# Optimization experiments

Measured on AMD Instinct MI355X. Metric: run time of the kernel, lower is better.

The kernel has to match this reference:

```python
import jax, jax.numpy as jnp
import numpy as np

N_NODES = 50000
N_EDGES = 800000


def sage_conv(x, src, dst, W_l, W_r, b):
    # PyG SAGEConv (mean aggr): out = lin_l(mean_{j->i} x_j) + lin_r(x_i)
    msg_sum = jax.ops.segment_sum(x[src], dst, num_segments=N_NODES)  # [N, d]
    deg = jax.ops.segment_sum(jnp.ones((src.shape[0],), x.dtype), dst,
                              num_segments=N_NODES)
    agg = msg_sum / jnp.clip(deg, 1.0)[:, None]
    return agg @ W_l.T + x @ W_r.T + b


def setup_inputs() -> dict:
    key = jax.random.key(0)
    ks = jax.random.split(key, 8)
    in_dim, hid, out_dim = 128, 256, 128
    x = jax.random.normal(ks[0], (N_NODES, in_dim), dtype=jnp.float32)
    edge_index = jax.random.randint(ks[1], (2, N_EDGES), 0, N_NODES, dtype=jnp.int64)
    s1 = 1.0 / np.sqrt(in_dim)
    s2 = 1.0 / np.sqrt(hid)
    return {
        "x": x,
        "edge_index": edge_index,
        "W_l1": jax.random.uniform(ks[2], (hid, in_dim), jnp.float32, -s1, s1),
        "W_r1": jax.random.uniform(ks[3], (hid, in_dim), jnp.float32, -s1, s1),
        "b1": jnp.zeros((hid,), jnp.float32),
        "W_l2": jax.random.uniform(ks[4], (out_dim, hid), jnp.float32, -s2, s2),
        "W_r2": jax.random.uniform(ks[5], (out_dim, hid), jnp.float32, -s2, s2),
        "b2": jnp.zeros((out_dim,), jnp.float32),
    }


def reference(x, edge_index, W_l1, W_r1, b1, W_l2, W_r2, b2):
    src, dst = edge_index[0], edge_index[1]
    h = sage_conv(x, src, dst, W_l1, W_r1, b1)
    h = jax.nn.relu(h)
    # dropout is identity in eval mode
    out = sage_conv(h, src, dst, W_l2, W_r2, b2)
    return out
```

## Files before the change

### kernel.cpp

```cpp
#include <hip/hip_runtime.h>

#define N_NODES 50000
#define N_EDGES 800000

typedef float f32x4 __attribute__((ext_vector_type(4)));
typedef _Float16 half4 __attribute__((ext_vector_type(4)));
typedef _Float16 half8 __attribute__((ext_vector_type(8)));
typedef int iv4 __attribute__((ext_vector_type(4)));

#define NPR 6250
#define CB 256
#define CAP 48

#define ZERO_BLOCKS ((N_NODES + 255) / 256)
#define CVT_BLOCKS ((N_NODES * 32 + 255) / 256)


__global__ __launch_bounds__(256) void setup_kernel(
    const float* __restrict__ x, _Float16* __restrict__ x16,
    const float* __restrict__ Wl1, const float* __restrict__ Wr1,
    const float* __restrict__ Wl2, const float* __restrict__ Wr2,
    _Float16* __restrict__ B1h, _Float16* __restrict__ B1l,
    _Float16* __restrict__ B2h, _Float16* __restrict__ B2l,
    int* __restrict__ counts) {
    int bid = blockIdx.x;
    int t = threadIdx.x;
    if (bid < ZERO_BLOCKS) {
        int i = bid * 256 + t;
        if (i < N_NODES) counts[i] = 0;
        return;
    }
    bid -= ZERO_BLOCKS;
    if (bid < 256) {
        int k = bid;
        int n = t;
        float v1 = (k < 128) ? Wl1[n * 128 + k] : Wr1[n * 128 + (k - 128)];
        float v2 = (n < 128) ? Wl2[n * 256 + k] : Wr2[(n - 128) * 256 + k];
        size_t fi = ((size_t)((k >> 5) * 16 + (n >> 4)) * 64 +
                     ((n & 15) + 16 * ((k & 31) >> 3))) * 8 + (k & 7);
        _Float16 h1 = (_Float16)v1;
        _Float16 h2 = (_Float16)v2;
        B1h[fi] = h1; B1l[fi] = (_Float16)(v1 - (float)h1);
        B2h[fi] = h2; B2l[fi] = (_Float16)(v2 - (float)h2);
        return;
    }
    bid -= 256;
    int i = bid * 256 + t;
    if (i < N_NODES * 32) {
        float4 v = reinterpret_cast<const float4*>(x)[i];
        half4 o = {(_Float16)v.x, (_Float16)v.y, (_Float16)v.z, (_Float16)v.w};
        reinterpret_cast<half4*>(x16)[i] = o;
    }
}


__global__ __launch_bounds__(256) void fill_kernel(const int* __restrict__ src,
                                                   const int* __restrict__ dst,
                                                   int* __restrict__ counts,
                                                   unsigned short* __restrict__ eidx, int E4) {
    int xcd = blockIdx.x & 7;
    int cb = blockIdx.x >> 3;
    int lo = xcd * NPR, hi = lo + NPR;
    int stride = (gridDim.x >> 3) * blockDim.x;
    const iv4* src4 = reinterpret_cast<const iv4*>(src);
    const iv4* dst4 = reinterpret_cast<const iv4*>(dst);
    for (int q = cb * blockDim.x + threadIdx.x; q < E4; q += stride) {
        iv4 d4 = __builtin_nontemporal_load(&dst4[q]);
        iv4 s4 = __builtin_nontemporal_load(&src4[q]);
#pragma unroll
        for (int u = 0; u < 4; u++) {
            int d = d4[u];
            if (d >= lo && d < hi) {
                int pos = atomicAdd(&counts[d], 1);
                if (pos < CAP) eidx[d * CAP + pos] = (unsigned short)s4[u];
            }
        }
    }
}


template <int OMODE>
__global__ __launch_bounds__(256) void gather_kernel(
    const unsigned short* __restrict__ eidx, const int* __restrict__ counts,
    const _Float16* __restrict__ xin, void* __restrict__ outp) {
    int wid = (blockIdx.x * 256 + threadIdx.x) >> 6;
    int lane = threadIdx.x & 63;
    if (wid >= N_NODES) return;
    int c = counts[wid];
    int end = c < CAP ? c : CAP;
    int base = wid * CAP;
    int half = lane >> 5;
    int c4 = lane & 31;
    float4 acc = {0, 0, 0, 0};
    int j = half;
    for (; j + 6 < end; j += 8) {
        int s0 = eidx[base + j],     s1 = eidx[base + j + 2];
        int s2 = eidx[base + j + 4], s3 = eidx[base + j + 6];
        half4 v0 = *reinterpret_cast<const half4*>(&xin[(size_t)s0 * 128 + c4 * 4]);
        half4 v1 = *reinterpret_cast<const half4*>(&xin[(size_t)s1 * 128 + c4 * 4]);
        half4 v2 = *reinterpret_cast<const half4*>(&xin[(size_t)s2 * 128 + c4 * 4]);
        half4 v3 = *reinterpret_cast<const half4*>(&xin[(size_t)s3 * 128 + c4 * 4]);
        acc.x += (float)v0.x + (float)v1.x + (float)v2.x + (float)v3.x;
        acc.y += (float)v0.y + (float)v1.y + (float)v2.y + (float)v3.y;
        acc.z += (float)v0.z + (float)v1.z + (float)v2.z + (float)v3.z;
        acc.w += (float)v0.w + (float)v1.w + (float)v2.w + (float)v3.w;
    }
    for (; j < end; j += 2) {
        int s0 = eidx[base + j];
        half4 v0 = *reinterpret_cast<const half4*>(&xin[(size_t)s0 * 128 + c4 * 4]);
        acc.x += (float)v0.x; acc.y += (float)v0.y; acc.z += (float)v0.z; acc.w += (float)v0.w;
    }
    acc.x += __shfl_xor(acc.x, 32);
    acc.y += __shfl_xor(acc.y, 32);
    acc.z += __shfl_xor(acc.z, 32);
    acc.w += __shfl_xor(acc.w, 32);
    if (half == 0) {
        float w = 1.0f / fmaxf((float)c, 1.0f);
        if (OMODE == 0) {
            half4 r = {(_Float16)(acc.x * w), (_Float16)(acc.y * w),
                       (_Float16)(acc.z * w), (_Float16)(acc.w * w)};
            *reinterpret_cast<half4*>(&((_Float16*)outp)[(size_t)wid * 128 + c4 * 4]) = r;
        } else {
            float* p = &((float*)outp)[(size_t)wid * 128 + c4 * 4];
            float4 old = *reinterpret_cast<float4*>(p);
            float4 r = {old.x + acc.x * w, old.y + acc.y * w,
                        old.z + acc.z * w, old.w + acc.w * w};
            *reinterpret_cast<float4*>(p) = r;
        }
    }
}

template <int MODE>
__global__ __launch_bounds__(512, 4) void mfma_gemm_kernel(
    const _Float16* __restrict__ A0, const _Float16* __restrict__ A1,
    const _Float16* __restrict__ Bh, const _Float16* __restrict__ Bl,
    const float* __restrict__ bias, void* __restrict__ O0v, float* __restrict__ O1) {
    __shared__ _Float16 lA[8][8][64][8];
    const int tid = threadIdx.x;
    const int lane = tid & 63;
    const int w = tid >> 6;
    const int wm = w >> 2, wn = w & 3;
    const int m0 = blockIdx.x * 128;
    const int nb0 = wn * 4;

    f32x4 acc[4][4];
#pragma unroll
    for (int i = 0; i < 4; i++)
#pragma unroll
        for (int j = 0; j < 4; j++) acc[i][j] = f32x4{0.f, 0.f, 0.f, 0.f};

    const int ms = tid >> 2;
    const int c0 = tid & 3;
    {
        int node = m0 + ms;
#pragma unroll
        for (int i = 0; i < 8; i++) {
            int c = c0 + 4 * i;
            const _Float16* Asrc;
            int koff;
            if (MODE == 0) {
                Asrc = (c < 16) ? A0 : A1;
                koff = (c & 15) * 8;
            } else {
                Asrc = A0;
                koff = c * 8;
            }
            half8 v = {0, 0, 0, 0, 0, 0, 0, 0};
            if (node < N_NODES)
                v = *reinterpret_cast<const half8*>(
                    &Asrc[(size_t)node * (MODE == 0 ? 128 : 256) + koff]);
            *reinterpret_cast<half8*>(&lA[c >> 2][ms >> 4][(ms & 15) + 16 * (c & 3)][0]) = v;
        }
    }
    __syncthreads();

    for (int kt = 0; kt < 8; kt++) {
        half8 ah[4];
#pragma unroll
        for (int mb = 0; mb < 4; mb++)
            ah[mb] = *reinterpret_cast<const half8*>(&lA[kt][wm * 4 + mb][lane][0]);
#pragma unroll
        for (int nb = 0; nb < 4; nb++) {
            size_t fi = ((size_t)(kt * 16 + nb0 + nb) * 64 + lane) * 8;
            half8 vh = *reinterpret_cast<const half8*>(&Bh[fi]);
            half8 vl = *reinterpret_cast<const half8*>(&Bl[fi]);
            __builtin_amdgcn_s_setprio(1);
#pragma unroll
            for (int mb = 0; mb < 4; mb++) {
                acc[mb][nb] = __builtin_amdgcn_mfma_f32_16x16x32_f16(ah[mb], vh, acc[mb][nb], 0, 0, 0);
                acc[mb][nb] = __builtin_amdgcn_mfma_f32_16x16x32_f16(ah[mb], vl, acc[mb][nb], 0, 0, 0);
            }
            __builtin_amdgcn_s_setprio(0);
        }
    }

#pragma unroll
    for (int mb = 0; mb < 4; mb++) {
        int rbase = m0 + wm * 64 + mb * 16 + ((lane >> 4) << 2);
#pragma unroll
        for (int nb = 0; nb < 4; nb++) {
            int col = wn * 64 + nb * 16 + (lane & 15);
#pragma unroll
            for (int r = 0; r < 4; r++) {
                int row = rbase + r;
                if (row >= N_NODES) continue;
                float vv = acc[mb][nb][r];
                if (MODE == 0) {
                    ((_Float16*)O0v)[(size_t)row * 256 + col] =
                        (_Float16)fmaxf(vv + bias[col], 0.0f);
                } else {
                    if (col < 128)
                        ((_Float16*)O0v)[(size_t)row * 128 + col] = (_Float16)vv;
                    else
                        O1[(size_t)row * 128 + (col - 128)] = vv + bias[col - 128];
                }
            }
        }
    }
}

extern "C" void kernel_launch(void* const* d_in, const int* in_sizes, int n_in,
                              void* d_out, int out_size, void* d_ws, size_t ws_size,
                              hipStream_t stream) {
    const float* x   = (const float*)d_in[0];
    const int*   ei  = (const int*)d_in[1];
    const float* Wl1 = (const float*)d_in[2];
    const float* Wr1 = (const float*)d_in[3];
    const float* b1  = (const float*)d_in[4];
    const float* Wl2 = (const float*)d_in[5];
    const float* Wr2 = (const float*)d_in[6];
    const float* b2  = (const float*)d_in[7];
    float* out = (float*)d_out;

    const int* srcp = ei;
    const int* dstp = ei + N_EDGES;

    int*            counts = (int*)d_ws;
    unsigned short* eidx   = (unsigned short*)(counts + N_NODES);
    _Float16*       B1h    = (_Float16*)(eidx + N_NODES * CAP);
    _Float16*       B1l    = B1h + 65536;
    _Float16*       B2h    = B1l + 65536;
    _Float16*       B2l    = B2h + 65536;
    _Float16*       agg16  = B2l + 65536;
    _Float16*       x16    = agg16 + (size_t)N_NODES * 128;
    _Float16*       h16    = x16 + (size_t)N_NODES * 128;
    _Float16*       z16    = agg16;

    setup_kernel<<<ZERO_BLOCKS + 256 + CVT_BLOCKS, 256, 0, stream>>>(
        x, x16, Wl1, Wr1, Wl2, Wr2, B1h, B1l, B2h, B2l, counts);
    fill_kernel<<<8 * CB, 256, 0, stream>>>(srcp, dstp, counts, eidx, N_EDGES / 4);

    int ggrid = (N_NODES + 127) / 128;

    gather_kernel<0><<<(N_NODES * 64 + 255) / 256, 256, 0, stream>>>(
        eidx, counts, x16, (void*)agg16);
    mfma_gemm_kernel<0><<<ggrid, 512, 0, stream>>>(agg16, x16, B1h, B1l, b1, (void*)h16, nullptr);

    mfma_gemm_kernel<1><<<ggrid, 512, 0, stream>>>(h16, nullptr, B2h, B2l, b2, (void*)z16, out);
    gather_kernel<1><<<(N_NODES * 64 + 255) / 256, 256, 0, stream>>>(
        eidx, counts, z16, (void*)out);
}
```

Before: 187.2 us.

## Replace global-atomic edge fill with two-pass partition and LDS bucketing

The adjacency build changes from one kernel doing a global atomicAdd per edge into two passes. First, each wave bins edges into 8 destination ranges using ballot-aggregated atomics and writes packed src/dst pairs to staging slots. Second, 64 blocks each build the adjacency for about 782 nodes in shared memory and copy counts and indices out with coalesced stores. This removes contended global atomics, but adds a staging round trip and a kernel launch, and the bucket pass runs on only 64 blocks, with each block scanning a whole bin's staging.

```diff
diff --git a/kernel.cpp b/kernel.cpp
--- a/kernel.cpp
+++ b/kernel.cpp
@@ -6,13 +6,13 @@
 typedef float f32x4 __attribute__((ext_vector_type(4)));
 typedef _Float16 half4 __attribute__((ext_vector_type(4)));
 typedef _Float16 half8 __attribute__((ext_vector_type(8)));
-typedef int iv4 __attribute__((ext_vector_type(4)));
 
 #define NPR 6250
-#define CB 256
+#define NPB 782
 #define CAP 48
-
-#define ZERO_BLOCKS ((N_NODES + 255) / 256)
+#define SUBCAP 16384
+#define PART_BLOCKS 1024
+
 #define CVT_BLOCKS ((N_NODES * 32 + 255) / 256)
 
 
@@ -22,15 +22,14 @@
     const float* __restrict__ Wl2, const float* __restrict__ Wr2,
     _Float16* __restrict__ B1h, _Float16* __restrict__ B1l,
     _Float16* __restrict__ B2h, _Float16* __restrict__ B2l,
-    int* __restrict__ counts) {
+    int* __restrict__ gcur) {
     int bid = blockIdx.x;
     int t = threadIdx.x;
-    if (bid < ZERO_BLOCKS) {
-        int i = bid * 256 + t;
-        if (i < N_NODES) counts[i] = 0;
+    if (bid == 0) {
+        if (t < 64) gcur[t] = 0;
         return;
     }
-    bid -= ZERO_BLOCKS;
+    bid -= 1;
     if (bid < 256) {
         int k = bid;
         int n = t;
@@ -54,28 +53,75 @@
 }
 
 
-__global__ __launch_bounds__(256) void fill_kernel(const int* __restrict__ src,
-                                                   const int* __restrict__ dst,
-                                                   int* __restrict__ counts,
-                                                   unsigned short* __restrict__ eidx, int E4) {
-    int xcd = blockIdx.x & 7;
-    int cb = blockIdx.x >> 3;
-    int lo = xcd * NPR, hi = lo + NPR;
-    int stride = (gridDim.x >> 3) * blockDim.x;
-    const iv4* src4 = reinterpret_cast<const iv4*>(src);
-    const iv4* dst4 = reinterpret_cast<const iv4*>(dst);
-    for (int q = cb * blockDim.x + threadIdx.x; q < E4; q += stride) {
-        iv4 d4 = __builtin_nontemporal_load(&dst4[q]);
-        iv4 s4 = __builtin_nontemporal_load(&src4[q]);
-#pragma unroll
-        for (int u = 0; u < 4; u++) {
-            int d = d4[u];
+__global__ __launch_bounds__(256) void fill_part_kernel(
+    const int* __restrict__ src, const int* __restrict__ dst,
+    int* __restrict__ gcur, unsigned int* __restrict__ staging, int E) {
+    int lane = threadIdx.x & 63;
+    int wg = ((blockIdx.x << 2) | (threadIdx.x >> 6)) & 7;
+    int stride = gridDim.x * blockDim.x;
+    int base = blockIdx.x * blockDim.x + (threadIdx.x & ~63);
+    for (; base < E; base += stride) {
+        int e = base + lane;
+        bool valid = e < E;
+        int d = valid ? dst[e] : 0;
+        int s = valid ? src[e] : 0;
+        int bin = valid ? d / NPR : 8;
+        unsigned int pk = ((unsigned int)s << 16) | (unsigned int)d;
+#pragma unroll
+        for (int b = 0; b < 8; b++) {
+            unsigned long long m = __ballot(bin == b);
+            if (m != 0ull) {
+                int leader = __ffsll((long long)m) - 1;
+                int total = __popcll(m);
+                int base_s = 0;
+                int cell = wg * 8 + b;
+                if (lane == leader) base_s = atomicAdd(&gcur[cell], total);
+                base_s = __shfl(base_s, leader);
+                if (bin == b) {
+                    int off = __popcll(m & ((1ull << lane) - 1ull));
+                    int slot = base_s + off;
+                    if (slot < SUBCAP)
+                        staging[(size_t)cell * SUBCAP + slot] = pk;
+                }
+            }
+        }
+    }
+}
+
+
+__global__ __launch_bounds__(256) void fill_bucket_kernel(
+    const unsigned int* __restrict__ staging, const int* __restrict__ gcur,
+    int* __restrict__ counts, unsigned short* __restrict__ eidx) {
+    __shared__ int lcnt[NPB];
+    __shared__ __align__(16) unsigned short lbuf[NPB * CAP];
+    int bin = blockIdx.x >> 3, sub = blockIdx.x & 7;
+    int lo = bin * NPR + sub * NPB;
+    int hi = lo + NPB;
+    int binend = (bin + 1) * NPR;
+    if (hi > binend) hi = binend;
+    int nn = hi - lo;
+    for (int i = threadIdx.x; i < nn; i += 256) lcnt[i] = 0;
+    __syncthreads();
+    for (int wg = 0; wg < 8; wg++) {
+        int cell = wg * 8 + bin;
+        int cnt = gcur[cell];
+        if (cnt > SUBCAP) cnt = SUBCAP;
+        const unsigned int* sp = staging + (size_t)cell * SUBCAP;
+        for (int i = threadIdx.x; i < cnt; i += 256) {
+            unsigned int pk = sp[i];
+            int d = (int)(pk & 0xffffu);
             if (d >= lo && d < hi) {
-                int pos = atomicAdd(&counts[d], 1);
-                if (pos < CAP) eidx[d * CAP + pos] = (unsigned short)s4[u];
-            }
-        }
-    }
+                int pos = atomicAdd(&lcnt[d - lo], 1);
+                if (pos < CAP) lbuf[(d - lo) * CAP + pos] = (unsigned short)(pk >> 16);
+            }
+        }
+    }
+    __syncthreads();
+    for (int i = threadIdx.x; i < nn; i += 256) counts[lo + i] = lcnt[i];
+    int n4 = (nn * CAP) >> 3;
+    const int4* lb4 = reinterpret_cast<const int4*>(lbuf);
+    int4* gb4 = reinterpret_cast<int4*>(eidx + (size_t)lo * CAP);
+    for (int i = threadIdx.x; i < n4; i += 256) gb4[i] = lb4[i];
 }
 
 
@@ -235,20 +281,23 @@
     const int* srcp = ei;
     const int* dstp = ei + N_EDGES;
 
-    int*            counts = (int*)d_ws;
-    unsigned short* eidx   = (unsigned short*)(counts + N_NODES);
-    _Float16*       B1h    = (_Float16*)(eidx + N_NODES * CAP);
-    _Float16*       B1l    = B1h + 65536;
-    _Float16*       B2h    = B1l + 65536;
-    _Float16*       B2l    = B2h + 65536;
-    _Float16*       agg16  = B2l + 65536;
-    _Float16*       x16    = agg16 + (size_t)N_NODES * 128;
-    _Float16*       h16    = x16 + (size_t)N_NODES * 128;
-    _Float16*       z16    = agg16;
-
-    setup_kernel<<<ZERO_BLOCKS + 256 + CVT_BLOCKS, 256, 0, stream>>>(
-        x, x16, Wl1, Wr1, Wl2, Wr2, B1h, B1l, B2h, B2l, counts);
-    fill_kernel<<<8 * CB, 256, 0, stream>>>(srcp, dstp, counts, eidx, N_EDGES / 4);
+    int*            counts  = (int*)d_ws;
+    unsigned short* eidx    = (unsigned short*)(counts + N_NODES);
+    unsigned int*   staging = (unsigned int*)(eidx + N_NODES * CAP);
+    int*            gcur    = (int*)(staging + 64 * SUBCAP);
+    _Float16*       B1h     = (_Float16*)(gcur + 64);
+    _Float16*       B1l     = B1h + 65536;
+    _Float16*       B2h     = B1l + 65536;
+    _Float16*       B2l     = B2h + 65536;
+    _Float16*       agg16   = B2l + 65536;
+    _Float16*       x16     = agg16 + (size_t)N_NODES * 128;
+    _Float16*       h16     = x16 + (size_t)N_NODES * 128;
+    _Float16*       z16     = agg16;
+
+    setup_kernel<<<1 + 256 + CVT_BLOCKS, 256, 0, stream>>>(
+        x, x16, Wl1, Wr1, Wl2, Wr2, B1h, B1l, B2h, B2l, gcur);
+    fill_part_kernel<<<PART_BLOCKS, 256, 0, stream>>>(srcp, dstp, gcur, staging, N_EDGES);
+    fill_bucket_kernel<<<64, 256, 0, stream>>>(staging, gcur, counts, eidx);
 
     int ggrid = (N_NODES + 127) / 128;
 
```

Measured after the change: 643.0 us (median of 2 runs). 3.44x slower.
